# Performance work log

Hardware: AMD Instinct MI355X
Metric: run time of the kernel (lower is better)

## Reference

```python
import jax, jax.numpy as jnp
import numpy as np


def setup_inputs() -> dict:
    key = jax.random.key(0)
    k1, k2, k3 = jax.random.split(key, 3)
    B, S, H, R, I = 4, 2048, 4096, 8, 11008
    return {
        "x": jax.random.normal(k1, (B, S, H), dtype=jnp.float32),
        "w1": jax.random.normal(k2, (2, H, R), dtype=jnp.float32),
        "w2": jax.random.normal(k3, (2, R, I), dtype=jnp.float32),
        "sparsity_pct": 50,  # sparsity = 0.50
    }


def reference(x, w1, w2, sparsity_pct):
    sparsity = sparsity_pct / 100.0
    H = x.shape[-1]
    I = w2.shape[-1]
    # flatten tokens: [N, H]; both branches share the same input (expand(2, ...))
    xt = x.reshape(-1, H)
    # low-rank projections per branch: [2, N, R] -> [2, N, I]
    p = jnp.einsum('nh,ghr->gnr', xt, w1)
    q = jnp.einsum('gnr,gri->gni', p, w2)
    # fused SiLU-gate: silu(branch0) * branch1 -> [N, I]
    g = jax.nn.silu(q[0]) * q[1]
    # L2 norm across tokens (dim=0) -> [I]
    n = jnp.sqrt(jnp.sum(g * g, axis=0))
    # top-k channel selection over intermediate_size
    k = int(I * (1.0 - sparsity))
    _, idx = jax.lax.top_k(n, k)
    return idx.reshape(-1)
```

## Files before the change

kernel.cpp:

```cpp
#include <hip/hip_runtime.h>
#include <stdint.h>

#define NTOK 8192
#define HDIM 4096
#define NI   11008

__global__ __launch_bounds__(512) void k1_proj(const float* __restrict__ x,
                                               const float* __restrict__ w1,
                                               float* __restrict__ p) {
    __shared__ double lds[8][64][16];
    const int tid = threadIdx.x;
    const int wv = __builtin_amdgcn_readfirstlane(tid >> 6);
    const int lane = tid & 63;
    const int token = blockIdx.x * 64 + lane;

    const float4* xr = (const float4*)(x + (size_t)token * HDIM + wv * 512);
    const float* wb = w1 + (size_t)wv * 512 * 8;

    double acc[16];
#pragma unroll
    for (int j = 0; j < 16; ++j) acc[j] = 0.0;

    for (int k4 = 0; k4 < 32; ++k4) {
        float4 a0 = xr[k4 * 4 + 0];
        float4 a1 = xr[k4 * 4 + 1];
        float4 a2 = xr[k4 * 4 + 2];
        float4 a3 = xr[k4 * 4 + 3];
        const float* w = wb + (size_t)k4 * 16 * 8;
        float xs[16] = {a0.x, a0.y, a0.z, a0.w, a1.x, a1.y, a1.z, a1.w,
                        a2.x, a2.y, a2.z, a2.w, a3.x, a3.y, a3.z, a3.w};
#pragma unroll
        for (int m = 0; m < 16; ++m) {
            double xd = (double)xs[m];
#pragma unroll
            for (int r = 0; r < 8; ++r) {
                acc[r]     = __fma_rn(xd, (double)w[m * 8 + r],         acc[r]);
                acc[8 + r] = __fma_rn(xd, (double)w[32768 + m * 8 + r], acc[8 + r]);
            }
        }
    }
#pragma unroll
    for (int j = 0; j < 16; ++j) lds[wv][lane][j] = acc[j];
    __syncthreads();
#pragma unroll
    for (int s = 0; s < 2; ++s) {
        int slot = tid + s * 512;
        int t = slot >> 4, j = slot & 15;
        double v = 0.0;
#pragma unroll
        for (int w = 0; w < 8; ++w) v += lds[w][t][j];
        p[((size_t)blockIdx.x * 64 + t) * 16 + j] = (float)v;
    }
}

__device__ __forceinline__ double g2_tok32(const float* __restrict__ pr,
                                           const float* waf, const float* wbf) {
    float q0 = 0.0f, q1 = 0.0f;
#pragma unroll
    for (int r = 0; r < 8; ++r) {
        q0 = __builtin_fmaf(pr[r],     waf[r], q0);
        q1 = __builtin_fmaf(pr[8 + r], wbf[r], q1);
    }
    float y = q0 * -1.44269504088896340736f;
    float ef;
    asm("v_exp_f32 %0, %1" : "=v"(ef) : "v"(y));
    float d = 1.0f + ef;
    float s = __builtin_amdgcn_rcpf(d);
    float g = (q0 * s) * q1;
    double gd = (double)g;
    return gd * gd;
}

__global__ __launch_bounds__(512, 4) void k2_nsq(const float* __restrict__ p,
                                                 const float* __restrict__ w2,
                                                 double* __restrict__ nsq_part) {
    __shared__ float  lds_p[256][20];
    __shared__ double lds_s[4][128];
    const int ib  = blockIdx.x % 86;
    const int c   = blockIdx.x / 86;
    const int ch  = threadIdx.x & 127;
    const int sub = threadIdx.x >> 7;
    const int i   = ib * 128 + ch;

    float waf[8], wbf[8];
#pragma unroll
    for (int r = 0; r < 8; ++r) {
        waf[r] = w2[(size_t)r * NI + i];
        wbf[r] = w2[(size_t)(8 + r) * NI + i];
    }
    double acc0 = 0.0, acc1 = 0.0;
    const int row = threadIdx.x >> 1;
    const int hf  = threadIdx.x & 1;
#pragma unroll 1
    for (int pass = 0; pass < 2; ++pass) {
        __syncthreads();
        {
            const float4* src = (const float4*)(p +
                ((size_t)c * 512 + pass * 256 + row) * 16 + hf * 8);
            float4 v0 = src[0], v1 = src[1];
            float4* dst = (float4*)&lds_p[row][hf * 8];
            dst[0] = v0;
            dst[1] = v1;
        }
        __syncthreads();
        const int t0 = sub * 64;
        for (int tl = t0; tl < t0 + 64; tl += 2) {
            acc0 = __fma_rn(1.0, g2_tok32(lds_p[tl],     waf, wbf), acc0);
            acc1 = __fma_rn(1.0, g2_tok32(lds_p[tl + 1], waf, wbf), acc1);
        }
    }
    __syncthreads();
    lds_s[sub][ch] = acc0 + acc1;
    __syncthreads();
    if (threadIdx.x < 128) {
        double s = 0.0;
#pragma unroll
        for (int q = 0; q < 4; ++q) s += lds_s[q][ch];
        nsq_part[(size_t)c * NI + i] = s;
    }
}

__device__ inline double dither_xi(unsigned int i, unsigned long long seed) {
    unsigned long long z = (unsigned long long)i * 0x9E3779B97F4A7C15ULL + seed;
    z = (z ^ (z >> 30)) * 0xBF58476D1CE4E5B9ULL;
    z = (z ^ (z >> 27)) * 0x94D049BB133111EBULL;
    z ^= z >> 31;
    return 2.0 * ((double)(z >> 11) * (1.0 / 9007199254740992.0)) - 1.0;
}

__global__ void k2b_key(const double* __restrict__ nsq_part,
                        unsigned long long* __restrict__ keys,
                        unsigned int* __restrict__ rank) {
    const int i = blockIdx.x * 256 + threadIdx.x;
    double s = 0.0, comp = 0.0;
#pragma unroll
    for (int c = 0; c < 16; ++c) {
        double yk = nsq_part[(size_t)c * NI + i] - comp;
        double tk = s + yk;
        comp = (tk - s) - yk;
        s = tk;
    }
    s = s * (1.0 + 2e-8 * dither_xi((unsigned int)i, 0x9E2025C0FFEE5EEDULL));
    float nf = (float)sqrt(s);
    unsigned int fb = __float_as_uint(nf);
    keys[i] = ((unsigned long long)fb << 32) |
              (unsigned long long)(0x0FFFFFFFu - (unsigned int)i);
    rank[i] = 0u;
}

__global__ __launch_bounds__(256) void k3_rank(const unsigned long long* __restrict__ keys,
                                               unsigned int* __restrict__ rank) {
    const int ib = blockIdx.x % 43;
    const int jc = blockIdx.x / 43;
    const int i  = ib * 256 + threadIdx.x;
    const unsigned long long ki = keys[i];
    unsigned int cnt = 0;
    const int j0 = jc * (NI / 32);
#pragma unroll 8
    for (int j = j0; j < j0 + NI / 32; ++j)
        cnt += (keys[j] > ki) ? 1u : 0u;
    if (cnt) atomicAdd(&rank[i], cnt);
}

__global__ void k4_scatter(const unsigned int* __restrict__ rank,
                           int* __restrict__ out, int k) {
    const int i = blockIdx.x * 256 + threadIdx.x;
    const unsigned int r = rank[i];
    if (r < (unsigned int)k) out[r] = (int)i;
}

extern "C" void kernel_launch(void* const* d_in, const int* in_sizes, int n_in,
                              void* d_out, int out_size, void* d_ws, size_t ws_size,
                              hipStream_t stream) {
    const float* x  = (const float*)d_in[0];
    const float* w1 = (const float*)d_in[1];
    const float* w2 = (const float*)d_in[2];
    char* ws = (char*)d_ws;
    float*              pbuf = (float*)(ws + 524288);
    double*             nsq  = (double*)(ws + 1572864);
    unsigned long long* keys = (unsigned long long*)(ws + 2981888);
    unsigned int*       rank = (unsigned int*)(ws + 3069952);
    int* out = (int*)d_out;

    hipLaunchKernelGGL(k1_proj,    dim3(128),     dim3(512), 0, stream, x, w1, pbuf);
    hipLaunchKernelGGL(k2_nsq,     dim3(86 * 16), dim3(512), 0, stream, pbuf, w2, nsq);
    hipLaunchKernelGGL(k2b_key,    dim3(43),      dim3(256), 0, stream, nsq, keys, rank);
    hipLaunchKernelGGL(k3_rank,    dim3(43 * 32), dim3(256), 0, stream, keys, rank);
    hipLaunchKernelGGL(k4_scatter, dim3(43),      dim3(256), 0, stream, rank, out, out_size);
}
```

Before: 160.4 us.

## Pre-convert w1 to double and split projection grid across branches

Adds a small kernel that converts w1 to fp64 once in workspace, so the projection kernel no longer converts weights per FMA. The projection kernel now launches 256 blocks, each handling one branch for 64 tokens instead of both, which doubles block count to fill more CUs on MI355X and halves per-thread accumulators. The trade-off is that x is read twice (once per branch), weight loads double in byte size, and there is an extra kernel launch.

```diff
diff --git a/kernel.cpp b/kernel.cpp
--- a/kernel.cpp
+++ b/kernel.cpp
@@ -5,51 +5,54 @@
 #define HDIM 4096
 #define NI   11008
 
+__global__ void k0_cvt(const float* __restrict__ w1, double* __restrict__ w1d) {
+    int i = blockIdx.x * 256 + threadIdx.x;
+    if (i < 2 * HDIM * 8) w1d[i] = (double)w1[i];
+}
+
 __global__ __launch_bounds__(512) void k1_proj(const float* __restrict__ x,
-                                               const float* __restrict__ w1,
+                                               const double* __restrict__ w1d,
                                                float* __restrict__ p) {
-    __shared__ double lds[8][64][16];
+    __shared__ double lds[8][64][8];
     const int tid = threadIdx.x;
     const int wv = __builtin_amdgcn_readfirstlane(tid >> 6);
     const int lane = tid & 63;
-    const int token = blockIdx.x * 64 + lane;
+    const int g  = blockIdx.x >> 7;
+    const int tg = blockIdx.x & 127;
+    const int token = tg * 64 + lane;
 
     const float4* xr = (const float4*)(x + (size_t)token * HDIM + wv * 512);
-    const float* wb = w1 + (size_t)wv * 512 * 8;
+    const double* wb = w1d + (size_t)g * 32768 + (size_t)wv * 512 * 8;
 
-    double acc[16];
+    double acc[8];
 #pragma unroll
-    for (int j = 0; j < 16; ++j) acc[j] = 0.0;
+    for (int j = 0; j < 8; ++j) acc[j] = 0.0;
 
     for (int k4 = 0; k4 < 32; ++k4) {
         float4 a0 = xr[k4 * 4 + 0];
         float4 a1 = xr[k4 * 4 + 1];
         float4 a2 = xr[k4 * 4 + 2];
         float4 a3 = xr[k4 * 4 + 3];
-        const float* w = wb + (size_t)k4 * 16 * 8;
+        const double* w = wb + (size_t)k4 * 16 * 8;
         float xs[16] = {a0.x, a0.y, a0.z, a0.w, a1.x, a1.y, a1.z, a1.w,
                         a2.x, a2.y, a2.z, a2.w, a3.x, a3.y, a3.z, a3.w};
 #pragma unroll
         for (int m = 0; m < 16; ++m) {
             double xd = (double)xs[m];
 #pragma unroll
-            for (int r = 0; r < 8; ++r) {
-                acc[r]     = __fma_rn(xd, (double)w[m * 8 + r],         acc[r]);
-                acc[8 + r] = __fma_rn(xd, (double)w[32768 + m * 8 + r], acc[8 + r]);
-            }
+            for (int r = 0; r < 8; ++r)
+                acc[r] = __fma_rn(xd, w[m * 8 + r], acc[r]);
         }
     }
 #pragma unroll
-    for (int j = 0; j < 16; ++j) lds[wv][lane][j] = acc[j];
+    for (int j = 0; j < 8; ++j) lds[wv][lane][j] = acc[j];
     __syncthreads();
-#pragma unroll
-    for (int s = 0; s < 2; ++s) {
-        int slot = tid + s * 512;
-        int t = slot >> 4, j = slot & 15;
+    {
+        int t = tid >> 3, j = tid & 7;
         double v = 0.0;
 #pragma unroll
         for (int w = 0; w < 8; ++w) v += lds[w][t][j];
-        p[((size_t)blockIdx.x * 64 + t) * 16 + j] = (float)v;
+        p[((size_t)tg * 64 + t) * 16 + g * 8 + j] = (float)v;
     }
 }
 
@@ -176,13 +179,15 @@
     const float* w1 = (const float*)d_in[1];
     const float* w2 = (const float*)d_in[2];
     char* ws = (char*)d_ws;
+    double*             w1d  = (double*)(ws + 0);
     float*              pbuf = (float*)(ws + 524288);
     double*             nsq  = (double*)(ws + 1572864);
     unsigned long long* keys = (unsigned long long*)(ws + 2981888);
     unsigned int*       rank = (unsigned int*)(ws + 3069952);
     int* out = (int*)d_out;
 
-    hipLaunchKernelGGL(k1_proj,    dim3(128),     dim3(512), 0, stream, x, w1, pbuf);
+    hipLaunchKernelGGL(k0_cvt,     dim3(256),     dim3(256), 0, stream, w1, w1d);
+    hipLaunchKernelGGL(k1_proj,    dim3(256),     dim3(512), 0, stream, x, w1d, pbuf);
     hipLaunchKernelGGL(k2_nsq,     dim3(86 * 16), dim3(512), 0, stream, pbuf, w2, nsq);
     hipLaunchKernelGGL(k2b_key,    dim3(43),      dim3(256), 0, stream, nsq, keys, rank);
     hipLaunchKernelGGL(k3_rank,    dim3(43 * 32), dim3(256), 0, stream, keys, rank);
```

Result: faster. 130.5 us (-18.7%).

## Split projection over hidden quarters, pre-convert w1 to double, read p directly

Applied to the files above, without the earlier changes.

The projection kernel now splits the hidden dimension into four chunks across 512 blocks instead of 128, which should fill more CUs. It writes double partials that a new combine kernel sums and rounds to float. A pre-pass converts w1 to double so the inner loop skips per-element float-to-double conversions. The norm kernel drops its LDS staging and barriers and reads p from global memory directly. This costs two extra launches and extra workspace traffic for the double partials.

```diff
diff --git a/kernel.cpp b/kernel.cpp
--- a/kernel.cpp
+++ b/kernel.cpp
@@ -5,28 +5,39 @@
 #define HDIM 4096
 #define NI   11008
 
-__global__ __launch_bounds__(512) void k1_proj(const float* __restrict__ x,
-                                               const float* __restrict__ w1,
-                                               float* __restrict__ p) {
+__global__ void k0_cvt(const float* __restrict__ w1, double* __restrict__ w1d) {
+    int i = blockIdx.x * 256 + threadIdx.x;
+    if (i < 2 * HDIM * 8) w1d[i] = (double)w1[i];
+}
+
+__global__ __launch_bounds__(512) void k1a_proj(const float* __restrict__ x,
+                                                const double* __restrict__ w1d,
+                                                double* __restrict__ p4) {
     __shared__ double lds[8][64][16];
     const int tid = threadIdx.x;
     const int wv = __builtin_amdgcn_readfirstlane(tid >> 6);
     const int lane = tid & 63;
-    const int token = blockIdx.x * 64 + lane;
+    const int hq = blockIdx.x >> 7;
+    const int tg = blockIdx.x & 127;
+    const int token = tg * 64 + lane;
+    const int hbase = hq * 1024 + wv * 128;
 
-    const float4* xr = (const float4*)(x + (size_t)token * HDIM + wv * 512);
-    const float* wb = w1 + (size_t)wv * 512 * 8;
+    const float4* xr = (const float4*)(x + (size_t)token * HDIM + hbase);
+    const double* wb0 = w1d + (size_t)hbase * 8;
+    const double* wb1 = w1d + 32768 + (size_t)hbase * 8;
 
     double acc[16];
 #pragma unroll
     for (int j = 0; j < 16; ++j) acc[j] = 0.0;
 
-    for (int k4 = 0; k4 < 32; ++k4) {
-        float4 a0 = xr[k4 * 4 + 0];
-        float4 a1 = xr[k4 * 4 + 1];
-        float4 a2 = xr[k4 * 4 + 2];
-        float4 a3 = xr[k4 * 4 + 3];
-        const float* w = wb + (size_t)k4 * 16 * 8;
+#pragma unroll 1
+    for (int it = 0; it < 8; ++it) {
+        float4 a0 = xr[it * 4 + 0];
+        float4 a1 = xr[it * 4 + 1];
+        float4 a2 = xr[it * 4 + 2];
+        float4 a3 = xr[it * 4 + 3];
+        const double* w0 = wb0 + (size_t)it * 16 * 8;
+        const double* w1p = wb1 + (size_t)it * 16 * 8;
         float xs[16] = {a0.x, a0.y, a0.z, a0.w, a1.x, a1.y, a1.z, a1.w,
                         a2.x, a2.y, a2.z, a2.w, a3.x, a3.y, a3.z, a3.w};
 #pragma unroll
@@ -34,8 +45,8 @@
             double xd = (double)xs[m];
 #pragma unroll
             for (int r = 0; r < 8; ++r) {
-                acc[r]     = __fma_rn(xd, (double)w[m * 8 + r],         acc[r]);
-                acc[8 + r] = __fma_rn(xd, (double)w[32768 + m * 8 + r], acc[8 + r]);
+                acc[r]     = __fma_rn(xd, w0[m * 8 + r],  acc[r]);
+                acc[8 + r] = __fma_rn(xd, w1p[m * 8 + r], acc[8 + r]);
             }
         }
     }
@@ -49,8 +60,15 @@
         double v = 0.0;
 #pragma unroll
         for (int w = 0; w < 8; ++w) v += lds[w][t][j];
-        p[((size_t)blockIdx.x * 64 + t) * 16 + j] = (float)v;
+        p4[(size_t)hq * (NTOK * 16) + ((size_t)tg * 64 + t) * 16 + j] = v;
     }
+}
+
+__global__ void k1b_comb(const double* __restrict__ p4, float* __restrict__ p) {
+    int i = blockIdx.x * 256 + threadIdx.x;
+    double v = p4[i] + p4[NTOK * 16 + i] + p4[2 * NTOK * 16 + i]
+             + p4[3 * NTOK * 16 + i];
+    p[i] = (float)v;
 }
 
 __device__ __forceinline__ double g2_tok32(const float* __restrict__ pr,
@@ -74,7 +92,6 @@
 __global__ __launch_bounds__(512, 4) void k2_nsq(const float* __restrict__ p,
                                                  const float* __restrict__ w2,
                                                  double* __restrict__ nsq_part) {
-    __shared__ float  lds_p[256][20];
     __shared__ double lds_s[4][128];
     const int ib  = blockIdx.x % 86;
     const int c   = blockIdx.x / 86;
@@ -89,27 +106,15 @@
         wbf[r] = w2[(size_t)(8 + r) * NI + i];
     }
     double acc0 = 0.0, acc1 = 0.0;
-    const int row = threadIdx.x >> 1;
-    const int hf  = threadIdx.x & 1;
 #pragma unroll 1
     for (int pass = 0; pass < 2; ++pass) {
-        __syncthreads();
-        {
-            const float4* src = (const float4*)(p +
-                ((size_t)c * 512 + pass * 256 + row) * 16 + hf * 8);
-            float4 v0 = src[0], v1 = src[1];
-            float4* dst = (float4*)&lds_p[row][hf * 8];
-            dst[0] = v0;
-            dst[1] = v1;
-        }
-        __syncthreads();
-        const int t0 = sub * 64;
-        for (int tl = t0; tl < t0 + 64; tl += 2) {
-            acc0 = __fma_rn(1.0, g2_tok32(lds_p[tl],     waf, wbf), acc0);
-            acc1 = __fma_rn(1.0, g2_tok32(lds_p[tl + 1], waf, wbf), acc1);
+        const float* pb = p + ((size_t)c * 512 + pass * 256 + sub * 64) * 16;
+#pragma unroll 2
+        for (int k = 0; k < 64; k += 2) {
+            acc0 = __fma_rn(1.0, g2_tok32(pb + (size_t)k * 16,       waf, wbf), acc0);
+            acc1 = __fma_rn(1.0, g2_tok32(pb + (size_t)(k + 1) * 16, waf, wbf), acc1);
         }
     }
-    __syncthreads();
     lds_s[sub][ch] = acc0 + acc1;
     __syncthreads();
     if (threadIdx.x < 128) {
@@ -176,13 +181,17 @@
     const float* w1 = (const float*)d_in[1];
     const float* w2 = (const float*)d_in[2];
     char* ws = (char*)d_ws;
+    double*             w1d  = (double*)(ws + 0);
     float*              pbuf = (float*)(ws + 524288);
     double*             nsq  = (double*)(ws + 1572864);
     unsigned long long* keys = (unsigned long long*)(ws + 2981888);
     unsigned int*       rank = (unsigned int*)(ws + 3069952);
+    double*             p4   = (double*)(ws + 4194304);
     int* out = (int*)d_out;
 
-    hipLaunchKernelGGL(k1_proj,    dim3(128),     dim3(512), 0, stream, x, w1, pbuf);
+    hipLaunchKernelGGL(k0_cvt,     dim3(256),     dim3(256), 0, stream, w1, w1d);
+    hipLaunchKernelGGL(k1a_proj,   dim3(512),     dim3(512), 0, stream, x, w1d, p4);
+    hipLaunchKernelGGL(k1b_comb,   dim3(512),     dim3(256), 0, stream, p4, pbuf);
     hipLaunchKernelGGL(k2_nsq,     dim3(86 * 16), dim3(512), 0, stream, pbuf, w2, nsq);
     hipLaunchKernelGGL(k2b_key,    dim3(43),      dim3(256), 0, stream, nsq, keys, rank);
     hipLaunchKernelGGL(k3_rank,    dim3(43 * 32), dim3(256), 0, stream, keys, rank);
```

Measured after the change: 244.4 us. +52.3%, slower.
